# Optimization experiments

Measured on AMD Instinct MI355X. Metric: run time of the kernel, lower is better.

The kernel has to match this reference:

```python
import jax, jax.numpy as jnp
import numpy as np


def layer_norm(x, w, b, eps=1e-5):
    mu = jnp.mean(x, axis=-1, keepdims=True)
    var = jnp.mean(jnp.square(x - mu), axis=-1, keepdims=True)
    return (x - mu) / jnp.sqrt(var + eps) * w + b


def setup_inputs() -> dict:
    B, T, S, D, K = 8, 2048, 2048, 512, 3
    ks = jax.random.split(jax.random.key(0), 8)
    w_scale = 0.02  # modest init so softmax/layernorm stay in a sane range
    return {
        "x": jax.random.normal(ks[0], (B, T, D), jnp.float32),
        "enc": jax.random.normal(ks[1], (B, S, D), jnp.float32),
        "conv_w": jax.random.normal(ks[2], (2 * D, D, K), jnp.float32) * w_scale,
        "conv_b": jnp.zeros((2 * D,), jnp.float32),
        "ln1_w": jnp.ones((D,), jnp.float32),
        "ln1_b": jnp.zeros((D,), jnp.float32),
        "Wq": jax.random.normal(ks[3], (D, D), jnp.float32) * w_scale,
        "bq": jnp.zeros((D,), jnp.float32),
        "Wk": jax.random.normal(ks[4], (D, D), jnp.float32) * w_scale,
        "bk": jnp.zeros((D,), jnp.float32),
        "Wv": jax.random.normal(ks[5], (D, D), jnp.float32) * w_scale,
        "bv": jnp.zeros((D,), jnp.float32),
        "Wo": jax.random.normal(ks[6], (D, D), jnp.float32) * w_scale,
        "bo": jnp.zeros((D,), jnp.float32),
        "ln2_w": jnp.ones((D,), jnp.float32),
        "ln2_b": jnp.zeros((D,), jnp.float32),
    }


def reference(x, enc, conv_w, conv_b, ln1_w, ln1_b, Wq, bq, Wk, bk, Wv, bv, Wo, bo, ln2_w, ln2_b):
    D = x.shape[-1]
    K = conv_w.shape[-1]
    # Causal GLU: left-pad by K-1 so each output sees only past/current positions.
    xt = jnp.transpose(x, (0, 2, 1))  # [B, D, T]
    xt = jnp.pad(xt, ((0, 0), (0, 0), (K - 1, 0)))
    conv = jax.lax.conv_general_dilated(
        xt, conv_w, window_strides=(1,), padding="VALID",
        dimension_numbers=("NCH", "OIH", "NCH"))
    conv = conv + conv_b[None, :, None]
    conv = jnp.transpose(conv, (0, 2, 1))  # [B, T, 2D]
    a, g = jnp.split(conv, 2, axis=-1)
    glu = a * jax.nn.sigmoid(g)
    # residual + LN1 (dropout is identity in eval mode)
    h = layer_norm(glu + x, ln1_w, ln1_b)
    # cross-attention: bmm -> softmax -> bmm (single head)
    q = h @ Wq.T + bq            # [B, T, D]
    k = enc @ Wk.T + bk          # [B, S, D]
    v = enc @ Wv.T + bv          # [B, S, D]
    scores = jnp.einsum("btd,bsd->bts", q, k) / jnp.sqrt(jnp.float32(D))
    attn = jax.nn.softmax(scores, axis=-1)  # [B, T, S]
    ctx = jnp.einsum("bts,bsd->btd", attn, v)
    ctx = ctx @ Wo.T + bo
    out = layer_norm(h + ctx, ln2_w, ln2_b)
    return out, attn
```

## Files before the change

kernel.cpp:

```cpp
#include <hip/hip_runtime.h>
#include <hip/hip_bf16.h>
#include <stdint.h>


typedef unsigned short ushortT;
typedef __bf16 bf16x8 __attribute__((ext_vector_type(8)));
typedef float floatx4 __attribute__((ext_vector_type(4)));
typedef unsigned short ushort4v __attribute__((ext_vector_type(4)));
typedef unsigned short ushort8 __attribute__((ext_vector_type(8)));

__device__ __forceinline__ ushortT f2bf(float f) {
  unsigned u = __builtin_bit_cast(unsigned, f);
  u += 0x7FFFu + ((u >> 16) & 1u);
  return (ushortT)(u >> 16);
}

__device__ __forceinline__ void gload_lds16(const void* g, void* l) {
  __builtin_amdgcn_global_load_lds(
      (const __attribute__((address_space(1))) void*)g,
      (__attribute__((address_space(3))) void*)l, 16, 0, 0);
}

__global__ __launch_bounds__(256)
void k_f32_to_bf16v(const float* __restrict__ src, ushortT* __restrict__ dst, long n4) {
  long i = (long)blockIdx.x * 256 + threadIdx.x;
  if (i >= n4) return;
  floatx4 v = *(const floatx4*)&src[i * 4];
  ushort4v o;
#pragma unroll
  for (int j = 0; j < 4; j++) o[j] = f2bf(v[j]);
  *(ushort4v*)&dst[i * 4] = o;
}

__global__ __launch_bounds__(128)
void k_xpad(const float* __restrict__ x, ushortT* __restrict__ xp) {
  int row = blockIdx.x;
  int b = row / 2050, tp = row % 2050;
  int c = threadIdx.x * 4;
  ushort4v o = {0, 0, 0, 0};
  if (tp >= 2) {
    floatx4 v = *(const floatx4*)&x[((long)(b * 2048 + tp - 2)) * 512 + c];
#pragma unroll
    for (int j = 0; j < 4; j++) o[j] = f2bf(v[j]);
  }
  *(ushort4v*)&xp[(long)row * 512 + c] = o;
}

__global__ __launch_bounds__(256)
void k_convw(const float* __restrict__ w, ushortT* __restrict__ dst) {
  long idx = (long)blockIdx.x * 256 + threadIdx.x;
  if (idx >= 1024L * 1536) return;
  int n = (int)(idx / 1536), kk = (int)(idx % 1536);
  int tap = kk >> 9, i = kk & 511;
  int o = ((n >> 4) & 1) * 512 + (n >> 5) * 16 + (n & 15);
  dst[idx] = f2bf(w[(o * 512 + i) * 3 + tap]);
}

template<int CONV_A, int BIAS, int GLU, int WBF16>
__global__ __launch_bounds__(256)
void k_gemm(const ushortT* __restrict__ A, long aBatch, int lda,
            const ushortT* __restrict__ Bm, long bBatch, int ldb,
            const float* __restrict__ bias, const float* __restrict__ xres,
            float* __restrict__ Cf, ushortT* __restrict__ Cb, long cBatch, int ldc,
            int Kdim, float scale)
{
  __shared__ ushortT As[128 * 32];
  __shared__ ushortT Bs[128 * 32];
  const int tid  = threadIdx.x;
  const int lane = tid & 63;
  const int wave = tid >> 6;
  const int wrow = (wave >> 1) * 64;
  const int wcol = (wave & 1) * 64;
  const int l15  = lane & 15;
  const int quad = lane >> 4;
  const long zA = (long)blockIdx.z * aBatch;
  const long zB = (long)blockIdx.z * bBatch;
  const long zC = (long)blockIdx.z * cBatch;
  const int rowBase = blockIdx.x * 128;
  const int colBase = blockIdx.y * 128;

  floatx4 zero = {0.f, 0.f, 0.f, 0.f};
  floatx4 acc[4][4];
#pragma unroll
  for (int mi = 0; mi < 4; mi++)
#pragma unroll
    for (int ni = 0; ni < 4; ni++) acc[mi][ni] = zero;

  for (int k0 = 0; k0 < Kdim; k0 += 32) {
    __syncthreads();
    {
      int ch = tid;
#pragma unroll
      for (int it = 0; it < 2; it++, ch += 256) {
        int row = ch >> 2, c8 = (ch & 3) << 3;
        if (CONV_A) {
          int gr = rowBase + row, gc = k0 + c8;
          int tap = gc >> 9, ii = gc & 511;
          int b = gr >> 11, t = gr & 2047;
          long gofs = ((long)(b * 2050 + t + tap) << 9) + ii;
          gload_lds16(A + gofs, &As[ch * 8]);
        } else {
          long gofs = zA + (long)(rowBase + row) * lda + (k0 + c8);
          gload_lds16(A + gofs, &As[ch * 8]);
        }
      }
      ch = tid;
#pragma unroll
      for (int it = 0; it < 2; it++, ch += 256) {
        int row = ch >> 2, c8 = (ch & 3) << 3;
        long gofs = zB + (long)(colBase + row) * ldb + (k0 + c8);
        gload_lds16(Bm + gofs, &Bs[ch * 8]);
      }
    }
    __syncthreads();
    bf16x8 av[4], bv[4];
#pragma unroll
    for (int mi = 0; mi < 4; mi++)
      av[mi] = *(const bf16x8*)&As[(wrow + mi * 16 + l15) * 32 + quad * 8];
#pragma unroll
    for (int ni = 0; ni < 4; ni++)
      bv[ni] = *(const bf16x8*)&Bs[(wcol + ni * 16 + l15) * 32 + quad * 8];
#pragma unroll
    for (int mi = 0; mi < 4; mi++)
#pragma unroll
      for (int ni = 0; ni < 4; ni++)
        acc[mi][ni] = __builtin_amdgcn_mfma_f32_16x16x32_bf16(av[mi], bv[ni], acc[mi][ni], 0, 0, 0);
  }

  if (GLU) {
#pragma unroll
    for (int mi = 0; mi < 4; mi++) {
#pragma unroll
      for (int ni = 0; ni < 4; ni += 2) {
        int colA = colBase + wcol + ni * 16;
        int d = (colA >> 5) * 16 + l15;
        float ba = bias[d], bg = bias[512 + d];
#pragma unroll
        for (int r = 0; r < 4; r++) {
          int grow = rowBase + wrow + mi * 16 + quad * 4 + r;
          float a = acc[mi][ni][r] + ba;
          float g = acc[mi][ni + 1][r] + bg;
          float val = a / (1.0f + __expf(-g)) + xres[(long)grow * 512 + d];
          Cf[(long)grow * 512 + d] = val;
        }
      }
    }
  } else {
#pragma unroll
    for (int mi = 0; mi < 4; mi++) {
#pragma unroll
      for (int ni = 0; ni < 4; ni++) {
        int gcol = colBase + wcol + ni * 16 + l15;
        float bcol = (BIAS == 1) ? bias[gcol] : 0.0f;
#pragma unroll
        for (int r = 0; r < 4; r++) {
          int grow = rowBase + wrow + mi * 16 + quad * 4 + r;
          float val = acc[mi][ni][r] * scale + bcol + ((BIAS == 2) ? bias[grow] : 0.0f);
          long off = zC + (long)grow * ldc + gcol;
          if (WBF16) Cb[off] = f2bf(val);
          else       Cf[off] = val;
        }
      }
    }
  }
}

__global__ __launch_bounds__(128)
void k_ln(const float* __restrict__ src, const float* __restrict__ w, const float* __restrict__ b,
          float* __restrict__ outf, ushortT* __restrict__ outb)
{
  __shared__ float s1[2], s2[2];
  long r = blockIdx.x;
  int tid = threadIdx.x;
  floatx4 v = *(const floatx4*)&src[r * 512 + tid * 4];
  float sum = v[0] + v[1] + v[2] + v[3];
  float ssq = v[0]*v[0] + v[1]*v[1] + v[2]*v[2] + v[3]*v[3];
#pragma unroll
  for (int off = 32; off; off >>= 1) { sum += __shfl_xor(sum, off); ssq += __shfl_xor(ssq, off); }
  if ((tid & 63) == 0) { s1[tid >> 6] = sum; s2[tid >> 6] = ssq; }
  __syncthreads();
  sum = s1[0] + s1[1]; ssq = s2[0] + s2[1];
  float mu = sum * (1.0f / 512.0f);
  float var = ssq * (1.0f / 512.0f) - mu * mu;
  float rstd = rsqrtf(var + 1e-5f);
  floatx4 wv = *(const floatx4*)&w[tid * 4];
  floatx4 bv = *(const floatx4*)&b[tid * 4];
  floatx4 o; ushort4v ob;
#pragma unroll
  for (int j = 0; j < 4; j++) { o[j] = (v[j] - mu) * rstd * wv[j] + bv[j]; ob[j] = f2bf(o[j]); }
  *(floatx4*)&outf[r * 512 + tid * 4] = o;
  *(ushort4v*)&outb[r * 512 + tid * 4] = ob;
}

__global__ __launch_bounds__(128)
void k_add_ln(const float* __restrict__ h, const float* __restrict__ c,
              const float* __restrict__ w, const float* __restrict__ b,
              float* __restrict__ out)
{
  __shared__ float s1[2], s2[2];
  long r = blockIdx.x;
  int tid = threadIdx.x;
  floatx4 v = *(const floatx4*)&h[r * 512 + tid * 4];
  floatx4 cv = *(const floatx4*)&c[r * 512 + tid * 4];
#pragma unroll
  for (int j = 0; j < 4; j++) v[j] += cv[j];
  float sum = v[0] + v[1] + v[2] + v[3];
  float ssq = v[0]*v[0] + v[1]*v[1] + v[2]*v[2] + v[3]*v[3];
#pragma unroll
  for (int off = 32; off; off >>= 1) { sum += __shfl_xor(sum, off); ssq += __shfl_xor(ssq, off); }
  if ((tid & 63) == 0) { s1[tid >> 6] = sum; s2[tid >> 6] = ssq; }
  __syncthreads();
  sum = s1[0] + s1[1]; ssq = s2[0] + s2[1];
  float mu = sum * (1.0f / 512.0f);
  float var = ssq * (1.0f / 512.0f) - mu * mu;
  float rstd = rsqrtf(var + 1e-5f);
  floatx4 wv = *(const floatx4*)&w[tid * 4];
  floatx4 bv = *(const floatx4*)&b[tid * 4];
  floatx4 o;
#pragma unroll
  for (int j = 0; j < 4; j++) o[j] = (v[j] - mu) * rstd * wv[j] + bv[j];
  *(floatx4*)&out[r * 512 + tid * 4] = o;
}

__global__ __launch_bounds__(256)
void k_softmax(float* __restrict__ attn, ushortT* __restrict__ attnbf)
{
  __shared__ float sred[4];
  long r = blockIdx.x;
  float* row = attn + r * 2048;
  ushortT* brow = attnbf + r * 2048;
  int tid = threadIdx.x;
  floatx4 v0 = *(const floatx4*)&row[tid * 4];
  floatx4 v1 = *(const floatx4*)&row[1024 + tid * 4];
  float mx = fmaxf(fmaxf(fmaxf(v0[0], v0[1]), fmaxf(v0[2], v0[3])),
                   fmaxf(fmaxf(v1[0], v1[1]), fmaxf(v1[2], v1[3])));
#pragma unroll
  for (int off = 32; off; off >>= 1) mx = fmaxf(mx, __shfl_xor(mx, off));
  if ((tid & 63) == 0) sred[tid >> 6] = mx;
  __syncthreads();
  mx = fmaxf(fmaxf(sred[0], sred[1]), fmaxf(sred[2], sred[3]));
  __syncthreads();
  float sum = 0.f;
#pragma unroll
  for (int j = 0; j < 4; j++) { v0[j] = __expf(v0[j] - mx); sum += v0[j]; }
#pragma unroll
  for (int j = 0; j < 4; j++) { v1[j] = __expf(v1[j] - mx); sum += v1[j]; }
#pragma unroll
  for (int off = 32; off; off >>= 1) sum += __shfl_xor(sum, off);
  if ((tid & 63) == 0) sred[tid >> 6] = sum;
  __syncthreads();
  sum = sred[0] + sred[1] + sred[2] + sred[3];
  float inv = 1.0f / sum;
  ushort4v b0, b1;
#pragma unroll
  for (int j = 0; j < 4; j++) { v0[j] *= inv; v1[j] *= inv; b0[j] = f2bf(v0[j]); b1[j] = f2bf(v1[j]); }
  *(floatx4*)&row[tid * 4] = v0;
  *(floatx4*)&row[1024 + tid * 4] = v1;
  *(ushort4v*)&brow[tid * 4] = b0;
  *(ushort4v*)&brow[1024 + tid * 4] = b1;
}

extern "C" void kernel_launch(void* const* d_in, const int* in_sizes, int n_in,
                              void* d_out, int out_size, void* d_ws, size_t ws_size,
                              hipStream_t stream)
{
  const float* x      = (const float*)d_in[0];
  const float* enc    = (const float*)d_in[1];
  const float* conv_w = (const float*)d_in[2];
  const float* conv_b = (const float*)d_in[3];
  const float* ln1_w  = (const float*)d_in[4];
  const float* ln1_b  = (const float*)d_in[5];
  const float* Wq     = (const float*)d_in[6];
  const float* bq     = (const float*)d_in[7];
  const float* Wk     = (const float*)d_in[8];
  const float* bk     = (const float*)d_in[9];
  const float* Wv     = (const float*)d_in[10];
  const float* bv     = (const float*)d_in[11];
  const float* Wo     = (const float*)d_in[12];
  const float* bo     = (const float*)d_in[13];
  const float* ln2_w  = (const float*)d_in[14];
  const float* ln2_b  = (const float*)d_in[15];

  const long BT = 16384, Dd = 512, S = 2048, TT = 2048;
  float* out  = (float*)d_out;
  float* attn = out + BT * Dd;

  char* p = (char*)d_ws;
  auto alloc = [&](size_t bytes) { char* r = p; p += (bytes + 255) & ~255UL; return r; };
  float*   hglu  = (float*)alloc(BT * Dd * 4);
  float*   h_f   = (float*)alloc(BT * Dd * 4);
  ushortT* xpad  = (ushortT*)alloc(8L * 2050 * 512 * 2);
  ushortT* encbf = (ushortT*)alloc(BT * Dd * 2);
  ushortT* hbf   = (ushortT*)alloc(BT * Dd * 2);
  ushortT* qbf   = (ushortT*)alloc(BT * Dd * 2);
  ushortT* kbf   = (ushortT*)alloc(BT * Dd * 2);
  ushortT* vT    = (ushortT*)alloc(Dd * BT * 2);
  ushortT* ctxbf = (ushortT*)alloc(BT * Dd * 2);
  ushortT* attnbf= (ushortT*)alloc(BT * S * 2);
  ushortT* Wcbf  = (ushortT*)alloc(1024L * 1536 * 2);
  ushortT* Wqbf  = (ushortT*)alloc(Dd * Dd * 2);
  ushortT* Wkbf  = (ushortT*)alloc(Dd * Dd * 2);
  ushortT* Wvbf  = (ushortT*)alloc(Dd * Dd * 2);
  ushortT* Wobf  = (ushortT*)alloc(Dd * Dd * 2);

  k_xpad<<<8 * 2050, 128, 0, stream>>>(x, xpad);
  k_f32_to_bf16v<<<(BT * Dd / 4 + 255) / 256, 256, 0, stream>>>(enc, encbf, BT * Dd / 4);
  k_convw<<<(1024 * 1536 + 255) / 256, 256, 0, stream>>>(conv_w, Wcbf);
  k_f32_to_bf16v<<<(Dd * Dd / 4 + 255) / 256, 256, 0, stream>>>(Wq, Wqbf, Dd * Dd / 4);
  k_f32_to_bf16v<<<(Dd * Dd / 4 + 255) / 256, 256, 0, stream>>>(Wk, Wkbf, Dd * Dd / 4);
  k_f32_to_bf16v<<<(Dd * Dd / 4 + 255) / 256, 256, 0, stream>>>(Wv, Wvbf, Dd * Dd / 4);
  k_f32_to_bf16v<<<(Dd * Dd / 4 + 255) / 256, 256, 0, stream>>>(Wo, Wobf, Dd * Dd / 4);

  k_gemm<1, 1, 1, 0><<<dim3(128, 8), 256, 0, stream>>>(
      xpad, 0, 0, Wcbf, 0, 1536, conv_b, x, hglu, nullptr, 0, 512, 1536, 1.0f);
  k_ln<<<16384, 128, 0, stream>>>(hglu, ln1_w, ln1_b, h_f, hbf);

  k_gemm<0, 1, 0, 1><<<dim3(128, 4), 256, 0, stream>>>(
      hbf, 0, 512, Wqbf, 0, 512, bq, nullptr, nullptr, qbf, 0, 512, 512, 1.0f);
  k_gemm<0, 1, 0, 1><<<dim3(128, 4), 256, 0, stream>>>(
      encbf, 0, 512, Wkbf, 0, 512, bk, nullptr, nullptr, kbf, 0, 512, 512, 1.0f);
  k_gemm<0, 2, 0, 1><<<dim3(4, 128), 256, 0, stream>>>(
      Wvbf, 0, 512, encbf, 0, 512, bv, nullptr, nullptr, vT, 0, 16384, 512, 1.0f);

  k_gemm<0, 0, 0, 0><<<dim3(16, 16, 8), 256, 0, stream>>>(
      qbf, TT * Dd, 512, kbf, S * Dd, 512, nullptr, nullptr,
      attn, nullptr, TT * S, 2048, 512, 0.04419417382415922f);
  k_softmax<<<16384, 256, 0, stream>>>(attn, attnbf);

  k_gemm<0, 0, 0, 1><<<dim3(16, 4, 8), 256, 0, stream>>>(
      attnbf, TT * S, 2048, vT, TT, 16384, nullptr, nullptr,
      nullptr, ctxbf, TT * Dd, 512, 2048, 1.0f);

  float* ctxo = hglu;
  k_gemm<0, 1, 0, 0><<<dim3(128, 4), 256, 0, stream>>>(
      ctxbf, 0, 512, Wobf, 0, 512, bo, nullptr, ctxo, nullptr, 0, 512, 512, 1.0f);
  k_add_ln<<<16384, 128, 0, stream>>>(h_f, ctxo, ln2_w, ln2_b, out);
}
```

Measured before the change: 609.3 us.

## Fuse output projection with LN2, store logits in bf16, merge weight casts

Several changes at once. The QK^T GEMM now writes bf16 logits instead of fp32, and softmax reads them and writes bf16 probabilities back in place for the PV GEMM, which cuts fp32 score traffic. The output projection, residual add and LayerNorm2 become one kernel working on 32-row tiles. The residual now comes from the bf16 copy of h, so the fp32 h buffer is dropped. The four weight casts are merged into one launch and the PV GEMM grid is swapped for better reuse. Rounding the logits and the residual to bf16 loses some accuracy.

```diff
diff --git a/kernel.cpp b/kernel.cpp
--- a/kernel.cpp
+++ b/kernel.cpp
@@ -14,6 +14,9 @@
   u += 0x7FFFu + ((u >> 16) & 1u);
   return (ushortT)(u >> 16);
 }
+__device__ __forceinline__ float bf2f(ushortT u) {
+  return __builtin_bit_cast(float, (unsigned)u << 16);
+}
 
 __device__ __forceinline__ void gload_lds16(const void* g, void* l) {
   __builtin_amdgcn_global_load_lds(
@@ -30,6 +33,21 @@
 #pragma unroll
   for (int j = 0; j < 4; j++) o[j] = f2bf(v[j]);
   *(ushort4v*)&dst[i * 4] = o;
+}
+
+__global__ __launch_bounds__(256)
+void k_w4(const float* __restrict__ w0, const float* __restrict__ w1,
+          const float* __restrict__ w2, const float* __restrict__ w3,
+          ushortT* __restrict__ dst) {
+  long i = (long)blockIdx.x * 256 + threadIdx.x;
+  int m = (int)(i >> 16);
+  long within = (i & 65535) * 4;
+  const float* s = (m == 0) ? w0 : (m == 1) ? w1 : (m == 2) ? w2 : w3;
+  floatx4 v = *(const floatx4*)&s[within];
+  ushort4v o;
+#pragma unroll
+  for (int j = 0; j < 4; j++) o[j] = f2bf(v[j]);
+  *(ushort4v*)&dst[(long)m * 262144 + within] = o;
 }
 
 __global__ __launch_bounds__(128)
@@ -56,7 +74,7 @@
   dst[idx] = f2bf(w[(o * 512 + i) * 3 + tap]);
 }
 
-template<int CONV_A, int BIAS, int GLU, int WBF16>
+template<int CONV_A, int BIAS, int GLU, int WBF16, int SWAP = 0>
 __global__ __launch_bounds__(256)
 void k_gemm(const ushortT* __restrict__ A, long aBatch, int lda,
             const ushortT* __restrict__ Bm, long bBatch, int ldb,
@@ -76,8 +94,8 @@
   const long zA = (long)blockIdx.z * aBatch;
   const long zB = (long)blockIdx.z * bBatch;
   const long zC = (long)blockIdx.z * cBatch;
-  const int rowBase = blockIdx.x * 128;
-  const int colBase = blockIdx.y * 128;
+  const int rowBase = (SWAP ? blockIdx.y : blockIdx.x) * 128;
+  const int colBase = (SWAP ? blockIdx.x : blockIdx.y) * 128;
 
   floatx4 zero = {0.f, 0.f, 0.f, 0.f};
   floatx4 acc[4][4];
@@ -167,7 +185,7 @@
 
 __global__ __launch_bounds__(128)
 void k_ln(const float* __restrict__ src, const float* __restrict__ w, const float* __restrict__ b,
-          float* __restrict__ outf, ushortT* __restrict__ outb)
+          ushortT* __restrict__ outb)
 {
   __shared__ float s1[2], s2[2];
   long r = blockIdx.x;
@@ -185,55 +203,27 @@
   float rstd = rsqrtf(var + 1e-5f);
   floatx4 wv = *(const floatx4*)&w[tid * 4];
   floatx4 bv = *(const floatx4*)&b[tid * 4];
-  floatx4 o; ushort4v ob;
-#pragma unroll
-  for (int j = 0; j < 4; j++) { o[j] = (v[j] - mu) * rstd * wv[j] + bv[j]; ob[j] = f2bf(o[j]); }
-  *(floatx4*)&outf[r * 512 + tid * 4] = o;
+  ushort4v ob;
+#pragma unroll
+  for (int j = 0; j < 4; j++) ob[j] = f2bf((v[j] - mu) * rstd * wv[j] + bv[j]);
   *(ushort4v*)&outb[r * 512 + tid * 4] = ob;
 }
 
-__global__ __launch_bounds__(128)
-void k_add_ln(const float* __restrict__ h, const float* __restrict__ c,
-              const float* __restrict__ w, const float* __restrict__ b,
-              float* __restrict__ out)
-{
-  __shared__ float s1[2], s2[2];
-  long r = blockIdx.x;
-  int tid = threadIdx.x;
-  floatx4 v = *(const floatx4*)&h[r * 512 + tid * 4];
-  floatx4 cv = *(const floatx4*)&c[r * 512 + tid * 4];
-#pragma unroll
-  for (int j = 0; j < 4; j++) v[j] += cv[j];
-  float sum = v[0] + v[1] + v[2] + v[3];
-  float ssq = v[0]*v[0] + v[1]*v[1] + v[2]*v[2] + v[3]*v[3];
-#pragma unroll
-  for (int off = 32; off; off >>= 1) { sum += __shfl_xor(sum, off); ssq += __shfl_xor(ssq, off); }
-  if ((tid & 63) == 0) { s1[tid >> 6] = sum; s2[tid >> 6] = ssq; }
-  __syncthreads();
-  sum = s1[0] + s1[1]; ssq = s2[0] + s2[1];
-  float mu = sum * (1.0f / 512.0f);
-  float var = ssq * (1.0f / 512.0f) - mu * mu;
-  float rstd = rsqrtf(var + 1e-5f);
-  floatx4 wv = *(const floatx4*)&w[tid * 4];
-  floatx4 bv = *(const floatx4*)&b[tid * 4];
-  floatx4 o;
-#pragma unroll
-  for (int j = 0; j < 4; j++) o[j] = (v[j] - mu) * rstd * wv[j] + bv[j];
-  *(floatx4*)&out[r * 512 + tid * 4] = o;
-}
-
-__global__ __launch_bounds__(256)
-void k_softmax(float* __restrict__ attn, ushortT* __restrict__ attnbf)
+__global__ __launch_bounds__(256)
+void k_softmax(ushortT* __restrict__ logits, float* __restrict__ attn)
 {
   __shared__ float sred[4];
   long r = blockIdx.x;
-  float* row = attn + r * 2048;
-  ushortT* brow = attnbf + r * 2048;
+  ushortT* lrow = logits + r * 2048;
+  float* arow = attn + r * 2048;
   int tid = threadIdx.x;
-  floatx4 v0 = *(const floatx4*)&row[tid * 4];
-  floatx4 v1 = *(const floatx4*)&row[1024 + tid * 4];
-  float mx = fmaxf(fmaxf(fmaxf(v0[0], v0[1]), fmaxf(v0[2], v0[3])),
-                   fmaxf(fmaxf(v1[0], v1[1]), fmaxf(v1[2], v1[3])));
+  ushort8 uv = *(const ushort8*)&lrow[tid * 8];
+  float v[8];
+#pragma unroll
+  for (int j = 0; j < 8; j++) v[j] = bf2f(uv[j]);
+  float mx = v[0];
+#pragma unroll
+  for (int j = 1; j < 8; j++) mx = fmaxf(mx, v[j]);
 #pragma unroll
   for (int off = 32; off; off >>= 1) mx = fmaxf(mx, __shfl_xor(mx, off));
   if ((tid & 63) == 0) sred[tid >> 6] = mx;
@@ -242,22 +232,112 @@
   __syncthreads();
   float sum = 0.f;
 #pragma unroll
-  for (int j = 0; j < 4; j++) { v0[j] = __expf(v0[j] - mx); sum += v0[j]; }
-#pragma unroll
-  for (int j = 0; j < 4; j++) { v1[j] = __expf(v1[j] - mx); sum += v1[j]; }
+  for (int j = 0; j < 8; j++) { v[j] = __expf(v[j] - mx); sum += v[j]; }
 #pragma unroll
   for (int off = 32; off; off >>= 1) sum += __shfl_xor(sum, off);
   if ((tid & 63) == 0) sred[tid >> 6] = sum;
   __syncthreads();
   sum = sred[0] + sred[1] + sred[2] + sred[3];
   float inv = 1.0f / sum;
-  ushort4v b0, b1;
-#pragma unroll
-  for (int j = 0; j < 4; j++) { v0[j] *= inv; v1[j] *= inv; b0[j] = f2bf(v0[j]); b1[j] = f2bf(v1[j]); }
-  *(floatx4*)&row[tid * 4] = v0;
-  *(floatx4*)&row[1024 + tid * 4] = v1;
-  *(ushort4v*)&brow[tid * 4] = b0;
-  *(ushort4v*)&brow[1024 + tid * 4] = b1;
+  floatx4 o0, o1;
+  ushort8 ob;
+#pragma unroll
+  for (int j = 0; j < 8; j++) {
+    float p = v[j] * inv;
+    if (j < 4) o0[j] = p; else o1[j - 4] = p;
+    ob[j] = f2bf(p);
+  }
+  *(floatx4*)&arow[tid * 8] = o0;
+  *(floatx4*)&arow[tid * 8 + 4] = o1;
+  *(ushort8*)&lrow[tid * 8] = ob;
+}
+
+__global__ __launch_bounds__(256)
+void k_oproj_ln(const ushortT* __restrict__ ctx, const ushortT* __restrict__ Wo,
+                const float* __restrict__ bo, const ushortT* __restrict__ h,
+                const float* __restrict__ w, const float* __restrict__ b,
+                float* __restrict__ out)
+{
+  __shared__ ushortT As[32 * 32];
+  __shared__ ushortT Bs[512 * 32];
+  __shared__ float psum[4][32], pssq[4][32];
+  const int tid = threadIdx.x, lane = tid & 63, wave = tid >> 6;
+  const int l15 = lane & 15, quad = lane >> 4;
+  const int rowBase = blockIdx.x * 32;
+
+  floatx4 zero = {0.f, 0.f, 0.f, 0.f};
+  floatx4 acc[2][8];
+#pragma unroll
+  for (int mi = 0; mi < 2; mi++)
+#pragma unroll
+    for (int ni = 0; ni < 8; ni++) acc[mi][ni] = zero;
+
+  for (int k0 = 0; k0 < 512; k0 += 32) {
+    __syncthreads();
+    if (tid < 128)
+      gload_lds16(ctx + (long)(rowBase + (tid >> 2)) * 512 + k0 + ((tid & 3) << 3), &As[tid * 8]);
+#pragma unroll
+    for (int it = 0; it < 8; it++) {
+      int ch = tid + it * 256;
+      gload_lds16(Wo + (long)(ch >> 2) * 512 + k0 + ((ch & 3) << 3), &Bs[ch * 8]);
+    }
+    __syncthreads();
+    bf16x8 av[2], bv[8];
+#pragma unroll
+    for (int mi = 0; mi < 2; mi++)
+      av[mi] = *(const bf16x8*)&As[(mi * 16 + l15) * 32 + quad * 8];
+#pragma unroll
+    for (int ni = 0; ni < 8; ni++)
+      bv[ni] = *(const bf16x8*)&Bs[(wave * 128 + ni * 16 + l15) * 32 + quad * 8];
+#pragma unroll
+    for (int mi = 0; mi < 2; mi++)
+#pragma unroll
+      for (int ni = 0; ni < 8; ni++)
+        acc[mi][ni] = __builtin_amdgcn_mfma_f32_16x16x32_bf16(av[mi], bv[ni], acc[mi][ni], 0, 0, 0);
+  }
+
+  float lnw[8], lnb[8], bov[8];
+#pragma unroll
+  for (int ni = 0; ni < 8; ni++) {
+    int col = wave * 128 + ni * 16 + l15;
+    bov[ni] = bo[col]; lnw[ni] = w[col]; lnb[ni] = b[col];
+  }
+#pragma unroll
+  for (int mi = 0; mi < 2; mi++) {
+#pragma unroll
+    for (int r = 0; r < 4; r++) {
+      long grow = rowBase + mi * 16 + quad * 4 + r;
+      float ps = 0.f, pq = 0.f;
+#pragma unroll
+      for (int ni = 0; ni < 8; ni++) {
+        int col = wave * 128 + ni * 16 + l15;
+        float val = acc[mi][ni][r] + bov[ni] + bf2f(h[grow * 512 + col]);
+        acc[mi][ni][r] = val;
+        ps += val; pq += val * val;
+      }
+#pragma unroll
+      for (int off = 1; off < 16; off <<= 1) { ps += __shfl_xor(ps, off); pq += __shfl_xor(pq, off); }
+      if (l15 == 0) { int rl = mi * 16 + quad * 4 + r; psum[wave][rl] = ps; pssq[wave][rl] = pq; }
+    }
+  }
+  __syncthreads();
+#pragma unroll
+  for (int mi = 0; mi < 2; mi++) {
+#pragma unroll
+    for (int r = 0; r < 4; r++) {
+      int rl = mi * 16 + quad * 4 + r;
+      float S = psum[0][rl] + psum[1][rl] + psum[2][rl] + psum[3][rl];
+      float Q = pssq[0][rl] + pssq[1][rl] + pssq[2][rl] + pssq[3][rl];
+      float mu = S * (1.0f / 512.0f);
+      float rstd = rsqrtf(Q * (1.0f / 512.0f) - mu * mu + 1e-5f);
+      long grow = rowBase + rl;
+#pragma unroll
+      for (int ni = 0; ni < 8; ni++) {
+        int col = wave * 128 + ni * 16 + l15;
+        out[grow * 512 + col] = (acc[mi][ni][r] - mu) * rstd * lnw[ni] + lnb[ni];
+      }
+    }
+  }
 }
 
 extern "C" void kernel_launch(void* const* d_in, const int* in_sizes, int n_in,
@@ -288,7 +368,6 @@
   char* p = (char*)d_ws;
   auto alloc = [&](size_t bytes) { char* r = p; p += (bytes + 255) & ~255UL; return r; };
   float*   hglu  = (float*)alloc(BT * Dd * 4);
-  float*   h_f   = (float*)alloc(BT * Dd * 4);
   ushortT* xpad  = (ushortT*)alloc(8L * 2050 * 512 * 2);
   ushortT* encbf = (ushortT*)alloc(BT * Dd * 2);
   ushortT* hbf   = (ushortT*)alloc(BT * Dd * 2);
@@ -296,24 +375,19 @@
   ushortT* kbf   = (ushortT*)alloc(BT * Dd * 2);
   ushortT* vT    = (ushortT*)alloc(Dd * BT * 2);
   ushortT* ctxbf = (ushortT*)alloc(BT * Dd * 2);
-  ushortT* attnbf= (ushortT*)alloc(BT * S * 2);
+  ushortT* sl    = (ushortT*)alloc(BT * S * 2);
   ushortT* Wcbf  = (ushortT*)alloc(1024L * 1536 * 2);
-  ushortT* Wqbf  = (ushortT*)alloc(Dd * Dd * 2);
-  ushortT* Wkbf  = (ushortT*)alloc(Dd * Dd * 2);
-  ushortT* Wvbf  = (ushortT*)alloc(Dd * Dd * 2);
-  ushortT* Wobf  = (ushortT*)alloc(Dd * Dd * 2);
+  ushortT* wall  = (ushortT*)alloc(4L * 262144 * 2);
+  ushortT* Wqbf = wall, *Wkbf = wall + 262144, *Wvbf = wall + 2 * 262144, *Wobf = wall + 3 * 262144;
 
   k_xpad<<<8 * 2050, 128, 0, stream>>>(x, xpad);
   k_f32_to_bf16v<<<(BT * Dd / 4 + 255) / 256, 256, 0, stream>>>(enc, encbf, BT * Dd / 4);
   k_convw<<<(1024 * 1536 + 255) / 256, 256, 0, stream>>>(conv_w, Wcbf);
-  k_f32_to_bf16v<<<(Dd * Dd / 4 + 255) / 256, 256, 0, stream>>>(Wq, Wqbf, Dd * Dd / 4);
-  k_f32_to_bf16v<<<(Dd * Dd / 4 + 255) / 256, 256, 0, stream>>>(Wk, Wkbf, Dd * Dd / 4);
-  k_f32_to_bf16v<<<(Dd * Dd / 4 + 255) / 256, 256, 0, stream>>>(Wv, Wvbf, Dd * Dd / 4);
-  k_f32_to_bf16v<<<(Dd * Dd / 4 + 255) / 256, 256, 0, stream>>>(Wo, Wobf, Dd * Dd / 4);
+  k_w4<<<1024, 256, 0, stream>>>(Wq, Wk, Wv, Wo, wall);
 
   k_gemm<1, 1, 1, 0><<<dim3(128, 8), 256, 0, stream>>>(
       xpad, 0, 0, Wcbf, 0, 1536, conv_b, x, hglu, nullptr, 0, 512, 1536, 1.0f);
-  k_ln<<<16384, 128, 0, stream>>>(hglu, ln1_w, ln1_b, h_f, hbf);
+  k_ln<<<16384, 128, 0, stream>>>(hglu, ln1_w, ln1_b, hbf);
 
   k_gemm<0, 1, 0, 1><<<dim3(128, 4), 256, 0, stream>>>(
       hbf, 0, 512, Wqbf, 0, 512, bq, nullptr, nullptr, qbf, 0, 512, 512, 1.0f);
@@ -322,17 +396,14 @@
   k_gemm<0, 2, 0, 1><<<dim3(4, 128), 256, 0, stream>>>(
       Wvbf, 0, 512, encbf, 0, 512, bv, nullptr, nullptr, vT, 0, 16384, 512, 1.0f);
 
-  k_gemm<0, 0, 0, 0><<<dim3(16, 16, 8), 256, 0, stream>>>(
+  k_gemm<0, 0, 0, 1><<<dim3(16, 16, 8), 256, 0, stream>>>(
       qbf, TT * Dd, 512, kbf, S * Dd, 512, nullptr, nullptr,
-      attn, nullptr, TT * S, 2048, 512, 0.04419417382415922f);
-  k_softmax<<<16384, 256, 0, stream>>>(attn, attnbf);
-
-  k_gemm<0, 0, 0, 1><<<dim3(16, 4, 8), 256, 0, stream>>>(
-      attnbf, TT * S, 2048, vT, TT, 16384, nullptr, nullptr,
+      nullptr, sl, TT * S, 2048, 512, 0.04419417382415922f);
+  k_softmax<<<16384, 256, 0, stream>>>(sl, attn);
+
+  k_gemm<0, 0, 0, 1, 1><<<dim3(4, 16, 8), 256, 0, stream>>>(
+      sl, TT * S, 2048, vT, TT, 16384, nullptr, nullptr,
       nullptr, ctxbf, TT * Dd, 512, 2048, 1.0f);
 
-  float* ctxo = hglu;
-  k_gemm<0, 1, 0, 0><<<dim3(128, 4), 256, 0, stream>>>(
-      ctxbf, 0, 512, Wobf, 0, 512, bo, nullptr, ctxo, nullptr, 0, 512, 512, 1.0f);
-  k_add_ln<<<16384, 128, 0, stream>>>(h_f, ctxo, ln2_w, ln2_b, out);
-}
+  k_oproj_ln<<<512, 256, 0, stream>>>(ctxbf, Wobf, bo, hbf, ln2_w, ln2_b, out);
+}
```

Result: faster. 587.9 us (-3.5%).
